# Performance work log

Hardware: AMD Instinct MI355X
Metric: run time of the kernel (lower is better)

Reference implementation:

```python
import jax, jax.numpy as jnp
import numpy as np

B, S, D_MODEL, H = 2, 2048, 1024, 16
DEPTH = D_MODEL // H


def setup_inputs() -> dict:
    key = jax.random.key(0)
    ks = jax.random.split(key, 12)
    s = 1.0 / np.sqrt(D_MODEL)
    inp = {
        "q": jax.random.normal(ks[0], (B, S, D_MODEL), jnp.float32),
        "k": jax.random.normal(ks[1], (B, S, D_MODEL), jnp.float32),
        "v": jax.random.normal(ks[2], (B, S, D_MODEL), jnp.float32),
        # CTRL-style causal mask: 1 where position is disallowed (future), 0 otherwise
        "mask": jnp.triu(jnp.ones((S, S), jnp.float32), k=1),
        "Wq_w": jax.random.normal(ks[3], (D_MODEL, D_MODEL), jnp.float32) * s,
        "Wq_b": jax.random.normal(ks[4], (D_MODEL,), jnp.float32) * s,
        "Wk_w": jax.random.normal(ks[5], (D_MODEL, D_MODEL), jnp.float32) * s,
        "Wk_b": jax.random.normal(ks[6], (D_MODEL,), jnp.float32) * s,
        "Wv_w": jax.random.normal(ks[7], (D_MODEL, D_MODEL), jnp.float32) * s,
        "Wv_b": jax.random.normal(ks[8], (D_MODEL,), jnp.float32) * s,
        "dense_w": jax.random.normal(ks[9], (D_MODEL, D_MODEL), jnp.float32) * s,
        "dense_b": jax.random.normal(ks[10], (D_MODEL,), jnp.float32) * s,
    }
    return inp


def _split_heads(x):
    # [B, S, D] -> [B, H, S, depth]
    b, s, _ = x.shape
    return x.reshape(b, s, H, DEPTH).transpose(0, 2, 1, 3)


def reference(q, k, v, mask, Wq_w, Wq_b, Wk_w, Wk_b, Wv_w, Wv_b, dense_w, dense_b):
    b = q.shape[0]
    # torch Linear: y = x @ W^T + b
    qh = _split_heads(q @ Wq_w.T + Wq_b)  # [B,H,Sq,dh]
    kh = _split_heads(k @ Wk_w.T + Wk_b)  # [B,H,Sk,dh]
    vh = _split_heads(v @ Wv_w.T + Wv_b)  # [B,H,Sk,dh]

    scale = 1.0 / np.sqrt(DEPTH)
    logits = jnp.einsum("bhqd,bhkd->bhqk", qh, kh) * scale  # [B,H,Sq,Sk]
    nd, ns = logits.shape[-2], logits.shape[-1]
    logits = logits + mask[ns - nd:ns, :ns] * -10000.0
    attn = jax.nn.softmax(logits, axis=-1)
    ctx = jnp.einsum("bhqk,bhkd->bhqd", attn, vh)  # [B,H,Sq,dh]
    ctx = ctx.transpose(0, 2, 1, 3).reshape(b, -1, D_MODEL)  # [B,Sq,D]
    out = ctx @ dense_w.T + dense_b
    return out
```

## Files before the change

kernel.cpp:

```cpp
#include <hip/hip_runtime.h>
#include <hip/hip_bf16.h>

typedef __bf16 bf16x8 __attribute__((ext_vector_type(8)));
typedef __bf16 bf16x4 __attribute__((ext_vector_type(4)));
typedef float  f32x4  __attribute__((ext_vector_type(4)));

#define D_MODEL 1024
#define SEQ     2048
#define NH      16
#define DH      64
#define MTOT    4096

__device__ __forceinline__ void gload16(const void* gp, void* lp) {
  __builtin_amdgcn_global_load_lds(
      (const __attribute__((address_space(1))) unsigned int*)gp,
      (__attribute__((address_space(3))) unsigned int*)lp,
      16, 0, 0);
}

struct CvtSegs {
  const float* s[7];
  __bf16*      d[7];
  int          n8[7];
};

__global__ __launch_bounds__(256) void cvt_kernel(CvtSegs c) {
  const int seg = blockIdx.y;
  const float4* s = (const float4*)c.s[seg];
  bf16x8*       d = (bf16x8*)c.d[seg];
  const int n8 = c.n8[seg];
  for (int i = blockIdx.x * 256 + threadIdx.x; i < n8; i += gridDim.x * 256) {
    float4 a = s[2 * i];
    float4 b = s[2 * i + 1];
    bf16x8 o;
    o[0] = (__bf16)a.x; o[1] = (__bf16)a.y; o[2] = (__bf16)a.z; o[3] = (__bf16)a.w;
    o[4] = (__bf16)b.x; o[5] = (__bf16)b.y; o[6] = (__bf16)b.z; o[7] = (__bf16)b.w;
    d[i] = o;
  }
}

template <int EPI>
__device__ __forceinline__ void gemm_core(const __bf16* __restrict__ A,
                                          const __bf16* __restrict__ W,
                                          const float* __restrict__ bias,
                                          void* __restrict__ outp,
                                          __bf16* Asm, __bf16* Bsm,
                                          int row0, int col0) {
  const int tid = threadIdx.x;
  const int lane = tid & 63;
  const int w = tid >> 6;
  const int lr = lane & 15, lg = lane >> 4;
  const int wr = w >> 1, wc = w & 1;
  char* AsB = (char*)Asm;
  char* BsB = (char*)Bsm;

  f32x4 acc[4][4];
#pragma unroll
  for (int i = 0; i < 4; ++i)
#pragma unroll
    for (int j = 0; j < 4; ++j) acc[i][j] = (f32x4){0.f, 0.f, 0.f, 0.f};

  for (int k0 = 0; k0 < D_MODEL; k0 += 64) {
#pragma unroll
    for (int i = 0; i < 4; ++i) {
      const int c0 = i * 4 + w;
      const int bo = c0 * 1024 + lane * 16;
      const int row = bo >> 7;
      const int gch = ((bo >> 4) & 7) ^ (row & 7);
      gload16(A + (size_t)(row0 + row) * D_MODEL + k0 + gch * 8, AsB + c0 * 1024);
      gload16(W + (size_t)(col0 + row) * D_MODEL + k0 + gch * 8, BsB + c0 * 1024);
    }
    __syncthreads();
#pragma unroll
    for (int kk = 0; kk < 2; ++kk) {
      bf16x8 af[4], bfr[4];
      const int kc = kk * 4 + lg;
#pragma unroll
      for (int mi = 0; mi < 4; ++mi) {
        const int row = wr * 64 + mi * 16 + lr;
        af[mi] = *(const bf16x8*)(AsB + row * 128 + ((kc ^ (row & 7)) << 4));
      }
#pragma unroll
      for (int ni = 0; ni < 4; ++ni) {
        const int col = wc * 64 + ni * 16 + lr;
        bfr[ni] = *(const bf16x8*)(BsB + col * 128 + ((kc ^ (col & 7)) << 4));
      }
#pragma unroll
      for (int mi = 0; mi < 4; ++mi)
#pragma unroll
        for (int ni = 0; ni < 4; ++ni)
          acc[mi][ni] = __builtin_amdgcn_mfma_f32_16x16x32_bf16(af[mi], bfr[ni],
                                                                acc[mi][ni], 0, 0, 0);
    }
    __syncthreads();
  }

#pragma unroll
  for (int mi = 0; mi < 4; ++mi) {
#pragma unroll
    for (int ni = 0; ni < 4; ++ni) {
      const int n = col0 + wc * 64 + ni * 16 + lr;
      const float bv = bias[n];
#pragma unroll
      for (int j = 0; j < 4; ++j) {
        const int m = row0 + wr * 64 + mi * 16 + lg * 4 + j;
        const float v = acc[mi][ni][j] + bv;
        if (EPI == 0) {
          __bf16* o = (__bf16*)outp;
          o[(size_t)((m >> 11) * NH + (n >> 6)) * (SEQ * DH) +
            (size_t)(m & 2047) * DH + (n & 63)] = (__bf16)v;
        } else {
          float* o = (float*)outp;
          o[(size_t)m * D_MODEL + n] = v;
        }
      }
    }
  }
}

struct QkvPtrs {
  const __bf16* A[3];
  const __bf16* W[3];
  const float*  b[3];
  __bf16*       o[3];
};

__global__ __launch_bounds__(256) void gemm_qkv_kernel(QkvPtrs p) {
  __shared__ __bf16 As[128 * 64];
  __shared__ __bf16 Bs[128 * 64];
  const int z = blockIdx.z;
  gemm_core<0>(p.A[z], p.W[z], p.b[z], p.o[z], As, Bs,
               blockIdx.x * 128, blockIdx.y * 128);
}

__global__ __launch_bounds__(256) void gemm_out_kernel(const __bf16* __restrict__ A,
                                                       const __bf16* __restrict__ W,
                                                       const float* __restrict__ b,
                                                       float* __restrict__ o) {
  __shared__ __bf16 As[128 * 64];
  __shared__ __bf16 Bs[128 * 64];
  gemm_core<1>(A, W, b, o, As, Bs, blockIdx.x * 128, blockIdx.y * 128);
}

__global__ __launch_bounds__(256, 4) void attn_kernel(const __bf16* __restrict__ qh,
                                                      const __bf16* __restrict__ kh,
                                                      const __bf16* __restrict__ vh,
                                                      __bf16* __restrict__ ctx) {
  __shared__ __bf16 Ks[2][64 * 64];
  __shared__ __bf16 Vt[2][64 * 64];
  __shared__ __bf16 Ps[4][16 * 64];

  const int bh = blockIdx.x;
  const int qb = 31 - blockIdx.y;
  const int tid = threadIdx.x, lane = tid & 63, w = tid >> 6;
  const int lr = lane & 15, lg = lane >> 4;
  const size_t hoff = (size_t)bh * SEQ * DH;
  const __bf16* Q  = qh + hoff;
  const __bf16* Kp = kh + hoff;
  const __bf16* Vp = vh + hoff;
  const int q0 = qb * 64 + w * 16;

  bf16x8 qf[2];
#pragma unroll
  for (int ki = 0; ki < 2; ++ki)
    qf[ki] = *(const bf16x8*)(Q + (size_t)(q0 + lr) * DH + ki * 32 + lg * 8);

  f32x4 o[4];
#pragma unroll
  for (int ni = 0; ni < 4; ++ni) o[ni] = (f32x4){0.f, 0.f, 0.f, 0.f};
  float lsum = 0.f;

  char* Psw = (char*)Ps[w];
  const int vkv = tid & 63;
  const int vd0 = (tid >> 6) * 8;
  const int nt = qb + 1;

#pragma unroll
  for (int s = 0; s < 2; ++s) {
    const int c = (w * 2 + s) * 64 + lane;
    const int row = c >> 3;
    const int gch = (c & 7) ^ (row & 7);
    gload16(Kp + (size_t)row * DH + gch * 8, (char*)Ks[0] + (w * 2 + s) * 1024);
  }
#pragma unroll
  for (int s = 0; s < 2; ++s) {
    const int d0 = vd0 + s * 32;
    bf16x8 vv = *(const bf16x8*)(Vp + (size_t)vkv * DH + d0);
#pragma unroll
    for (int i = 0; i < 8; ++i) {
      const int d = d0 + i;
      Vt[0][d * 64 + ((((vkv >> 3) ^ (d & 7)) << 3) | (vkv & 7))] = vv[i];
    }
  }

  int cur = 0;
  for (int t = 0; t < nt; ++t) {
    __syncthreads();
    const bool pf = (t + 1 < nt);
    bf16x8 vreg[2];
    if (pf) {
      const int nxt = cur ^ 1;
#pragma unroll
      for (int s = 0; s < 2; ++s) {
        const int c = (w * 2 + s) * 64 + lane;
        const int row = c >> 3;
        const int gch = (c & 7) ^ (row & 7);
        gload16(Kp + (size_t)((t + 1) * 64 + row) * DH + gch * 8,
                (char*)Ks[nxt] + (w * 2 + s) * 1024);
      }
#pragma unroll
      for (int s = 0; s < 2; ++s)
        vreg[s] = *(const bf16x8*)(Vp + (size_t)((t + 1) * 64 + vkv) * DH +
                                   vd0 + s * 32);
    }
    {
      char* KsB = (char*)Ks[cur];
      char* VtB = (char*)Vt[cur];

      f32x4 st[4];
#pragma unroll
      for (int ni = 0; ni < 4; ++ni) st[ni] = (f32x4){0.f, 0.f, 0.f, 0.f};
      __builtin_amdgcn_s_setprio(1);
#pragma unroll
      for (int ki = 0; ki < 2; ++ki) {
        const int kc = ki * 4 + lg;
#pragma unroll
        for (int ni = 0; ni < 4; ++ni) {
          const int row = ni * 16 + lr;
          bf16x8 kf = *(const bf16x8*)(KsB + row * 128 + ((kc ^ (row & 7)) << 4));
          st[ni] = __builtin_amdgcn_mfma_f32_16x16x32_bf16(kf, qf[ki], st[ni], 0, 0, 0);
        }
      }
      __builtin_amdgcn_s_setprio(0);

      const int kvb = t * 64;
      const bool needmask = (kvb + 63 > q0);
      const int q = q0 + lr;
      float p[4][4];
      float psum = 0.f;
#pragma unroll
      for (int ni = 0; ni < 4; ++ni) {
#pragma unroll
        for (int j = 0; j < 4; ++j) {
          float v = st[ni][j] * 0.18033688f;
          if (needmask && (kvb + ni * 16 + lg * 4 + j > q)) v = -1e9f;
          const float pe = exp2f(v);
          p[ni][j] = pe;
          psum += pe;
        }
      }
      lsum += psum;

#pragma unroll
      for (int ni = 0; ni < 4; ++ni) {
        bf16x4 pk;
#pragma unroll
        for (int j = 0; j < 4; ++j) pk[j] = (__bf16)p[ni][j];
        const int chunk = 2 * ni + (lg >> 1);
        *(bf16x4*)(Psw + lr * 128 + ((chunk ^ (lr & 7)) << 4) + (lg & 1) * 8) = pk;
      }
      asm volatile("s_waitcnt lgkmcnt(0)" ::: "memory");
      __builtin_amdgcn_sched_barrier(0);

      __builtin_amdgcn_s_setprio(1);
#pragma unroll
      for (int ki = 0; ki < 2; ++ki) {
        const int kc = ki * 4 + lg;
        bf16x8 pf2 = *(const bf16x8*)(Psw + lr * 128 + ((kc ^ (lr & 7)) << 4));
#pragma unroll
        for (int ni = 0; ni < 4; ++ni) {
          const int d = ni * 16 + lr;
          bf16x8 vf = *(const bf16x8*)(VtB + d * 128 + ((kc ^ (lr & 7)) << 4));
          o[ni] = __builtin_amdgcn_mfma_f32_16x16x32_bf16(pf2, vf, o[ni], 0, 0, 0);
        }
      }
      __builtin_amdgcn_s_setprio(0);
    }
    if (pf) {
      const int nxt = cur ^ 1;
#pragma unroll
      for (int s = 0; s < 2; ++s) {
        const int d0 = vd0 + s * 32;
#pragma unroll
        for (int i = 0; i < 8; ++i) {
          const int d = d0 + i;
          Vt[nxt][d * 64 + ((((vkv >> 3) ^ (d & 7)) << 3) | (vkv & 7))] = vreg[s][i];
        }
      }
    }
    cur ^= 1;
  }

  lsum += __shfl_xor(lsum, 16, 64);
  lsum += __shfl_xor(lsum, 32, 64);
  const int bb = bh >> 4, hh = bh & 15;
#pragma unroll
  for (int j = 0; j < 4; ++j) {
    const int row = lg * 4 + j;
    const float inv = 1.0f / __shfl(lsum, row, 64);
    const int qrow = q0 + row;
    __bf16* orow = ctx + (size_t)(bb * SEQ + qrow) * D_MODEL + hh * DH;
#pragma unroll
    for (int ni = 0; ni < 4; ++ni)
      orow[ni * 16 + lr] = (__bf16)(o[ni][j] * inv);
  }
}

extern "C" void kernel_launch(void* const* d_in, const int* in_sizes, int n_in,
                              void* d_out, int out_size, void* d_ws, size_t ws_size,
                              hipStream_t stream) {
  (void)in_sizes; (void)n_in; (void)out_size; (void)ws_size;
  const float* q  = (const float*)d_in[0];
  const float* k  = (const float*)d_in[1];
  const float* v  = (const float*)d_in[2];
  const float* Wq = (const float*)d_in[4];
  const float* bq = (const float*)d_in[5];
  const float* Wk = (const float*)d_in[6];
  const float* bk = (const float*)d_in[7];
  const float* Wv = (const float*)d_in[8];
  const float* bv = (const float*)d_in[9];
  const float* Wd = (const float*)d_in[10];
  const float* bd = (const float*)d_in[11];

  char* ws = (char*)d_ws;
  __bf16* qb  = (__bf16*)(ws + 0);
  __bf16* kb  = (__bf16*)(ws + 8388608);
  __bf16* vb  = (__bf16*)(ws + 16777216);
  __bf16* wqb = (__bf16*)(ws + 25165824);
  __bf16* wkb = (__bf16*)(ws + 27262976);
  __bf16* wvb = (__bf16*)(ws + 29360128);
  __bf16* wdb = (__bf16*)(ws + 31457280);
  __bf16* qhp = (__bf16*)(ws + 33554432);
  __bf16* khp = (__bf16*)(ws + 41943040);
  __bf16* vhp = (__bf16*)(ws + 50331648);
  __bf16* ctxp= (__bf16*)(ws + 58720256);

  CvtSegs cs;
  cs.s[0] = q;  cs.d[0] = qb;  cs.n8[0] = 524288;
  cs.s[1] = k;  cs.d[1] = kb;  cs.n8[1] = 524288;
  cs.s[2] = v;  cs.d[2] = vb;  cs.n8[2] = 524288;
  cs.s[3] = Wq; cs.d[3] = wqb; cs.n8[3] = 131072;
  cs.s[4] = Wk; cs.d[4] = wkb; cs.n8[4] = 131072;
  cs.s[5] = Wv; cs.d[5] = wvb; cs.n8[5] = 131072;
  cs.s[6] = Wd; cs.d[6] = wdb; cs.n8[6] = 131072;
  cvt_kernel<<<dim3(256, 7, 1), dim3(256), 0, stream>>>(cs);

  QkvPtrs qp;
  qp.A[0] = qb;  qp.A[1] = kb;  qp.A[2] = vb;
  qp.W[0] = wqb; qp.W[1] = wkb; qp.W[2] = wvb;
  qp.b[0] = bq;  qp.b[1] = bk;  qp.b[2] = bv;
  qp.o[0] = qhp; qp.o[1] = khp; qp.o[2] = vhp;
  gemm_qkv_kernel<<<dim3(32, 8, 3), dim3(256), 0, stream>>>(qp);

  attn_kernel<<<dim3(32, 32, 1), dim3(256), 0, stream>>>(qhp, khp, vhp, ctxp);

  gemm_out_kernel<<<dim3(32, 8, 1), dim3(256), 0, stream>>>(ctxp, wdb, bd, (float*)d_out);
}
```

Measured before the change: 133.5 us.

## Write V pre-transposed from QKV GEMM and async-load it into LDS

The V projection epilogue now writes V in a per-head transposed [dh, S] layout with packed 4-element bf16 stores. The attention kernel can then fetch V tiles with direct global-to-LDS async loads, like K, instead of loading into registers and scattering element-wise transposed writes into shared memory. The exp2 call is also replaced with the hardware exp2 builtin. The cost is strided global stores in the V GEMM epilogue, and the exp2 builtin may be less accurate.

```diff
diff --git a/kernel.cpp b/kernel.cpp
--- a/kernel.cpp
+++ b/kernel.cpp
@@ -95,23 +95,41 @@
     __syncthreads();
   }
 
-#pragma unroll
-  for (int mi = 0; mi < 4; ++mi) {
-#pragma unroll
-    for (int ni = 0; ni < 4; ++ni) {
-      const int n = col0 + wc * 64 + ni * 16 + lr;
-      const float bv = bias[n];
-#pragma unroll
-      for (int j = 0; j < 4; ++j) {
-        const int m = row0 + wr * 64 + mi * 16 + lg * 4 + j;
-        const float v = acc[mi][ni][j] + bv;
-        if (EPI == 0) {
-          __bf16* o = (__bf16*)outp;
-          o[(size_t)((m >> 11) * NH + (n >> 6)) * (SEQ * DH) +
-            (size_t)(m & 2047) * DH + (n & 63)] = (__bf16)v;
-        } else {
-          float* o = (float*)outp;
-          o[(size_t)m * D_MODEL + n] = v;
+  if (EPI == 2) {
+    __bf16* o = (__bf16*)outp;
+#pragma unroll
+    for (int mi = 0; mi < 4; ++mi) {
+#pragma unroll
+      for (int ni = 0; ni < 4; ++ni) {
+        const int n = col0 + wc * 64 + ni * 16 + lr;
+        const float bv = bias[n];
+        const int m0 = row0 + wr * 64 + mi * 16 + lg * 4;
+        bf16x4 pk;
+#pragma unroll
+        for (int j = 0; j < 4; ++j) pk[j] = (__bf16)(acc[mi][ni][j] + bv);
+        *(bf16x4*)(o + ((size_t)((m0 >> 11) * NH + (n >> 6)) * DH + (n & 63)) * SEQ +
+                   (m0 & 2047)) = pk;
+      }
+    }
+  } else {
+#pragma unroll
+    for (int mi = 0; mi < 4; ++mi) {
+#pragma unroll
+      for (int ni = 0; ni < 4; ++ni) {
+        const int n = col0 + wc * 64 + ni * 16 + lr;
+        const float bv = bias[n];
+#pragma unroll
+        for (int j = 0; j < 4; ++j) {
+          const int m = row0 + wr * 64 + mi * 16 + lg * 4 + j;
+          const float v = acc[mi][ni][j] + bv;
+          if (EPI == 0) {
+            __bf16* o = (__bf16*)outp;
+            o[(size_t)((m >> 11) * NH + (n >> 6)) * (SEQ * DH) +
+              (size_t)(m & 2047) * DH + (n & 63)] = (__bf16)v;
+          } else {
+            float* o = (float*)outp;
+            o[(size_t)m * D_MODEL + n] = v;
+          }
         }
       }
     }
@@ -129,8 +147,12 @@
   __shared__ __bf16 As[128 * 64];
   __shared__ __bf16 Bs[128 * 64];
   const int z = blockIdx.z;
-  gemm_core<0>(p.A[z], p.W[z], p.b[z], p.o[z], As, Bs,
-               blockIdx.x * 128, blockIdx.y * 128);
+  if (z == 2)
+    gemm_core<2>(p.A[z], p.W[z], p.b[z], p.o[z], As, Bs,
+                 blockIdx.x * 128, blockIdx.y * 128);
+  else
+    gemm_core<0>(p.A[z], p.W[z], p.b[z], p.o[z], As, Bs,
+                 blockIdx.x * 128, blockIdx.y * 128);
 }
 
 __global__ __launch_bounds__(256) void gemm_out_kernel(const __bf16* __restrict__ A,
@@ -144,7 +166,7 @@
 
 __global__ __launch_bounds__(256, 4) void attn_kernel(const __bf16* __restrict__ qh,
                                                       const __bf16* __restrict__ kh,
-                                                      const __bf16* __restrict__ vh,
+                                                      const __bf16* __restrict__ vt,
                                                       __bf16* __restrict__ ctx) {
   __shared__ __bf16 Ks[2][64 * 64];
   __shared__ __bf16 Vt[2][64 * 64];
@@ -155,9 +177,9 @@
   const int tid = threadIdx.x, lane = tid & 63, w = tid >> 6;
   const int lr = lane & 15, lg = lane >> 4;
   const size_t hoff = (size_t)bh * SEQ * DH;
-  const __bf16* Q  = qh + hoff;
-  const __bf16* Kp = kh + hoff;
-  const __bf16* Vp = vh + hoff;
+  const __bf16* Q   = qh + hoff;
+  const __bf16* Kp  = kh + hoff;
+  const __bf16* Vtp = vt + hoff;
   const int q0 = qb * 64 + w * 16;
 
   bf16x8 qf[2];
@@ -171,8 +193,6 @@
   float lsum = 0.f;
 
   char* Psw = (char*)Ps[w];
-  const int vkv = tid & 63;
-  const int vd0 = (tid >> 6) * 8;
   const int nt = qb + 1;
 
 #pragma unroll
@@ -181,24 +201,13 @@
     const int row = c >> 3;
     const int gch = (c & 7) ^ (row & 7);
     gload16(Kp + (size_t)row * DH + gch * 8, (char*)Ks[0] + (w * 2 + s) * 1024);
-  }
-#pragma unroll
-  for (int s = 0; s < 2; ++s) {
-    const int d0 = vd0 + s * 32;
-    bf16x8 vv = *(const bf16x8*)(Vp + (size_t)vkv * DH + d0);
-#pragma unroll
-    for (int i = 0; i < 8; ++i) {
-      const int d = d0 + i;
-      Vt[0][d * 64 + ((((vkv >> 3) ^ (d & 7)) << 3) | (vkv & 7))] = vv[i];
-    }
+    gload16(Vtp + (size_t)row * SEQ + gch * 8, (char*)Vt[0] + (w * 2 + s) * 1024);
   }
 
   int cur = 0;
   for (int t = 0; t < nt; ++t) {
     __syncthreads();
-    const bool pf = (t + 1 < nt);
-    bf16x8 vreg[2];
-    if (pf) {
+    if (t + 1 < nt) {
       const int nxt = cur ^ 1;
 #pragma unroll
       for (int s = 0; s < 2; ++s) {
@@ -207,11 +216,9 @@
         const int gch = (c & 7) ^ (row & 7);
         gload16(Kp + (size_t)((t + 1) * 64 + row) * DH + gch * 8,
                 (char*)Ks[nxt] + (w * 2 + s) * 1024);
-      }
-#pragma unroll
-      for (int s = 0; s < 2; ++s)
-        vreg[s] = *(const bf16x8*)(Vp + (size_t)((t + 1) * 64 + vkv) * DH +
-                                   vd0 + s * 32);
+        gload16(Vtp + (size_t)row * SEQ + (t + 1) * 64 + gch * 8,
+                (char*)Vt[nxt] + (w * 2 + s) * 1024);
+      }
     }
     {
       char* KsB = (char*)Ks[cur];
@@ -244,7 +251,7 @@
         for (int j = 0; j < 4; ++j) {
           float v = st[ni][j] * 0.18033688f;
           if (needmask && (kvb + ni * 16 + lg * 4 + j > q)) v = -1e9f;
-          const float pe = exp2f(v);
+          const float pe = __builtin_amdgcn_exp2f(v);
           p[ni][j] = pe;
           psum += pe;
         }
@@ -275,18 +282,6 @@
         }
       }
       __builtin_amdgcn_s_setprio(0);
-    }
-    if (pf) {
-      const int nxt = cur ^ 1;
-#pragma unroll
-      for (int s = 0; s < 2; ++s) {
-        const int d0 = vd0 + s * 32;
-#pragma unroll
-        for (int i = 0; i < 8; ++i) {
-          const int d = d0 + i;
-          Vt[nxt][d * 64 + ((((vkv >> 3) ^ (d & 7)) << 3) | (vkv & 7))] = vreg[s][i];
-        }
-      }
     }
     cur ^= 1;
   }
@@ -332,7 +327,7 @@
   __bf16* wdb = (__bf16*)(ws + 31457280);
   __bf16* qhp = (__bf16*)(ws + 33554432);
   __bf16* khp = (__bf16*)(ws + 41943040);
-  __bf16* vhp = (__bf16*)(ws + 50331648);
+  __bf16* vtp = (__bf16*)(ws + 50331648);
   __bf16* ctxp= (__bf16*)(ws + 58720256);
 
   CvtSegs cs;
@@ -349,10 +344,10 @@
   qp.A[0] = qb;  qp.A[1] = kb;  qp.A[2] = vb;
   qp.W[0] = wqb; qp.W[1] = wkb; qp.W[2] = wvb;
   qp.b[0] = bq;  qp.b[1] = bk;  qp.b[2] = bv;
-  qp.o[0] = qhp; qp.o[1] = khp; qp.o[2] = vhp;
+  qp.o[0] = qhp; qp.o[1] = khp; qp.o[2] = vtp;
   gemm_qkv_kernel<<<dim3(32, 8, 3), dim3(256), 0, stream>>>(qp);
 
-  attn_kernel<<<dim3(32, 32, 1), dim3(256), 0, stream>>>(qhp, khp, vhp, ctxp);
+  attn_kernel<<<dim3(32, 32, 1), dim3(256), 0, stream>>>(qhp, khp, vtp, ctxp);
 
   gemm_out_kernel<<<dim3(32, 8, 1), dim3(256), 0, stream>>>(ctxp, wdb, bd, (float*)d_out);
 }
```

After: 123.5 us. 7.5% less time.
